# Kernel tuning notes

Measured on AMD Instinct MI355X. Metric: run time of the kernel, lower is better.

The kernel has to match this reference:

```python
import jax, jax.numpy as jnp
import numpy as np

S, E, K, D = 50000, 20000, 128, 128  # students, exercises, knowledge, emb dim
NE = 800000                          # edges per polarity
B = 8192                             # batch of response logs
L = 3                                # gcn layers
TEMP, CONTROL = 0.2, 0.3


def setup_inputs() -> dict:
    key = jax.random.key(0)
    ks = jax.random.split(key, 40)

    def nrm(i, shape, scale=0.05):
        return jax.random.normal(ks[i], shape, jnp.float32) * scale

    def uni(i, shape):
        return jax.random.uniform(ks[i], shape, jnp.float32)

    inp = {
        'stu_id': jax.random.randint(ks[0], (B,), 0, S, jnp.int32),
        'exer_id': jax.random.randint(ks[1], (B,), 0, E, jnp.int32),
        'kn_emb': uni(2, (B, K)),
        'ui1_u': jax.random.randint(ks[3], (NE,), 0, S, jnp.int32),
        'ui1_i': jax.random.randint(ks[4], (NE,), 0, E, jnp.int32),
        'ui1_val': uni(5, (NE,)), 'iu1_val': uni(6, (NE,)),
        'eps_ui1': uni(7, (NE,)), 'eps_iu1': uni(8, (NE,)),
        'ui0_u': jax.random.randint(ks[9], (NE,), 0, S, jnp.int32),
        'ui0_i': jax.random.randint(ks[10], (NE,), 0, E, jnp.int32),
        'ui0_val': uni(11, (NE,)), 'iu0_val': uni(12, (NE,)),
        'eps_ui0': uni(13, (NE,)), 'eps_iu0': uni(14, (NE,)),
        # embeddings
        'student_emb': nrm(15, (S, D)), 'exercise_emb': nrm(16, (E, D)),
        'knowledge_emb': nrm(17, (K, D)),
        'stu_b': nrm(18, (S, 1)), 'exer_b': nrm(19, (E, 1)), 'disc': nrm(20, (E, 1)),
        # edge-gate MLPs (polarity 1 and 0)
        'W1_l1': nrm(21, (D, 2 * D)), 'b1_l1': jnp.zeros((D,), jnp.float32),
        'W2_l1': nrm(22, (1, D)), 'b2_l1': jnp.zeros((1,), jnp.float32),
        'W1_l0': nrm(23, (D, 2 * D)), 'b1_l0': jnp.zeros((D,), jnp.float32),
        'W2_l0': nrm(24, (1, D)), 'b2_l0': jnp.zeros((1,), jnp.float32),
        # PosLinear prednet
        'pw1': nrm(25, (256, K)), 'pb1': jnp.zeros((256,), jnp.float32),
        'pw2': nrm(26, (128, 256)), 'pb2': jnp.zeros((128,), jnp.float32),
        'pw3': nrm(27, (1, 128)), 'pb3': jnp.zeros((1,), jnp.float32),
    }
    return inp


def _gate(uids, iids, uemb, iemb, W1, b1, W2, b2, eps):
    # concrete-distribution edge gate; embeddings are detached in original code
    row = jax.lax.stop_gradient(uemb)[uids]          # [NE, D]
    col = jax.lax.stop_gradient(iemb)[iids]          # [NE, D]
    h = jax.nn.relu(jnp.concatenate([row, col], axis=1) @ W1.T + b1)
    logit = (h @ W2.T + b2).reshape(-1)              # [NE]
    eps = jnp.clip(eps, 1e-6, 1.0 - 1e-6)
    g = jnp.log(eps) - jnp.log1p(-eps)               # logistic noise
    return CONTROL * jax.nn.sigmoid((logit + g) / TEMP) + (1.0 - CONTROL)


def _spmm(rows, cols, vals, x, n_rows):
    # out[rows] += vals * x[cols]
    return jax.ops.segment_sum(vals[:, None] * x[cols], rows, num_segments=n_rows)


def _poslin(x, W, b):
    Wp = 2.0 * jax.nn.relu(-W) + W  # == |W|
    return x @ Wp.T + b


def reference(stu_id, exer_id, kn_emb, ui1_u, ui1_i, ui1_val, iu1_val, eps_ui1,
              eps_iu1, ui0_u, ui0_i, ui0_val, iu0_val, eps_ui0, eps_iu0,
              student_emb, exercise_emb, knowledge_emb, stu_b, exer_b, disc,
              W1_l1, b1_l1, W2_l1, b2_l1, W1_l0, b1_l0, W2_l0, b2_l0,
              pw1, pb1, pw2, pb2, pw3, pb3):
    # --- graph_learner: per-edge gates on all 4 sparse matrices ---
    v_ui1 = ui1_val * _gate(ui1_u, ui1_i, student_emb, exercise_emb, W1_l1, b1_l1, W2_l1, b2_l1, eps_ui1)
    v_iu1 = iu1_val * _gate(ui1_u, ui1_i, student_emb, exercise_emb, W1_l1, b1_l1, W2_l1, b2_l1, eps_iu1)
    v_ui0 = ui0_val * _gate(ui0_u, ui0_i, student_emb, exercise_emb, W1_l0, b1_l0, W2_l0, b2_l0, eps_ui0)
    v_iu0 = iu0_val * _gate(ui0_u, ui0_i, student_emb, exercise_emb, W1_l0, b1_l0, W2_l0, b2_l0, eps_iu0)

    # --- graph_representations: L rounds of sparse propagation, mean over layers ---
    stu, exer = student_emb, exercise_emb
    stu_sum, exer_sum = stu, exer
    for _ in range(L):
        u1 = _spmm(ui1_u, ui1_i, v_ui1, exer, S)
        i1 = _spmm(ui1_i, ui1_u, v_iu1, stu, E)
        u0 = _spmm(ui0_u, ui0_i, v_ui0, exer, S)
        i0 = _spmm(ui0_i, ui0_u, v_iu0, stu, E)
        stu, exer = u1 + u0, i1 + i0
        stu_sum = stu_sum + stu
        exer_sum = exer_sum + exer
    stu_final = stu_sum / (L + 1)
    exer_final = exer_sum / (L + 1)

    # --- NCDM-style prediction head with PosLinear MLP ---
    stat = jax.nn.sigmoid(stu_final[stu_id] @ knowledge_emb.T + stu_b[stu_id])   # [B, K]
    diff = jax.nn.sigmoid(exer_final[exer_id] @ knowledge_emb.T + exer_b[exer_id])
    e_d = jax.nn.sigmoid(disc[exer_id])                                          # [B, 1]
    x = e_d * (stat - diff) * kn_emb
    h = jax.nn.sigmoid(_poslin(x, pw1, pb1))
    h = jax.nn.sigmoid(_poslin(h, pw2, pb2))
    out = jax.nn.sigmoid(_poslin(h, pw3, pb3)).reshape(-1)                       # [B]
    return out
```

## Files before the change

kernel.cpp:

```cpp
#include <hip/hip_runtime.h>
#include <hip/hip_bf16.h>
#include <math.h>

#define S_N 50000
#define E_N 20000
#define K_N 128
#define D_N 128
#define NE_N 800000
#define B_N 8192
#define L_N 3
#define GATE_TILES (NE_N / 64)
#define NB_S 782
#define NB_E 313
#define BPAD 464
#define BSLACK 480

typedef __attribute__((ext_vector_type(4))) float floatx4;
typedef __attribute__((ext_vector_type(8))) short short8v;

__device__ __forceinline__ unsigned short f2bf(float x) {
  unsigned int u = __float_as_uint(x);
  u += 0x7FFFu + ((u >> 16) & 1u);
  return (unsigned short)(u >> 16);
}
__device__ __forceinline__ float bf2f(unsigned short u) {
  return __uint_as_float(((unsigned int)u) << 16);
}
__device__ __forceinline__ float sigm(float z) { return 1.0f / (1.0f + __expf(-z)); }

__device__ __forceinline__ unsigned char f2e4m3(float x) {
  unsigned int u = __float_as_uint(x);
  unsigned char s = (unsigned char)((u >> 24) & 0x80);
  int e = (int)((u >> 23) & 0xFF) - 127;
  unsigned int m = u & 0x7FFFFF;
  if (((u >> 23) & 0xFF) == 0) return s;
  if (e >= 9) return s | 0x7E;
  if (e < -10) return s;
  if (e >= -6) {
    unsigned int keep = m >> 20;
    unsigned int rest = m & 0xFFFFF;
    if (rest > 0x80000u || (rest == 0x80000u && (keep & 1))) keep++;
    if (keep == 8) { keep = 0; e++; if (e >= 9) return s | 0x7E; }
    unsigned char b = (unsigned char)(s | ((e + 7) << 3) | keep);
    if ((b & 0x7F) == 0x7F) b = s | 0x7E;
    return b;
  }
  int shift = -6 - e;
  unsigned int full = 0x800000u | m;
  unsigned int q = full >> (20 + shift);
  unsigned int rest = full & ((1u << (20 + shift)) - 1);
  unsigned int half = 1u << (19 + shift);
  if (rest > half || (rest == half && (q & 1))) q++;
  if (q == 8) return s | 0x08;
  return (unsigned char)(s | q);
}
__device__ __forceinline__ unsigned int pk4_fp8(float4 v) {
  return (unsigned int)f2e4m3(v.x) | ((unsigned int)f2e4m3(v.y) << 8) |
         ((unsigned int)f2e4m3(v.z) << 16) | ((unsigned int)f2e4m3(v.w) << 24);
}

__global__ void prep_kernel(const float* __restrict__ W1_l1, const float* __restrict__ W1_l0,
                            const float* __restrict__ pw1, const float* __restrict__ pw2,
                            const float* __restrict__ pw3, const float* __restrict__ ke,
                            unsigned int* __restrict__ w1f8_1, unsigned int* __restrict__ w1f8_0,
                            float* __restrict__ pw1T, float* __restrict__ pw2T,
                            float* __restrict__ pw3a, float* __restrict__ keT) {
  int i = blockIdx.x * blockDim.x + threadIdx.x;
  if (i < 8192) { w1f8_1[i] = pk4_fp8(((const float4*)W1_l1)[i]); return; }
  i -= 8192;
  if (i < 8192) { w1f8_0[i] = pk4_fp8(((const float4*)W1_l0)[i]); return; }
  i -= 8192;
  if (i < 32768) { int d = i >> 8, j = i & 255; pw1T[i] = fabsf(pw1[j * 128 + d]); return; }
  i -= 32768;
  if (i < 32768) { int d = i >> 7, j = i & 127; pw2T[i] = fabsf(pw2[j * 256 + d]); return; }
  i -= 32768;
  if (i < 128) { pw3a[i] = fabsf(pw3[i]); return; }
  i -= 128;
  if (i < 16384) { int d = i >> 7, k = i & 127; keT[i] = ke[k * 128 + d]; return; }
}

__global__ void init_bf_kernel(const float* __restrict__ se, const float* __restrict__ ee,
                               unsigned short* __restrict__ sbf, unsigned short* __restrict__ ebf,
                               unsigned int* __restrict__ sf8, unsigned int* __restrict__ ef8,
                               float* __restrict__ sS, float* __restrict__ eS) {
  int i = blockIdx.x * blockDim.x + threadIdx.x;
  const int nS4 = S_N * 32, nE4 = E_N * 32;
  if (i < nS4) {
    float4 v = ((const float4*)se)[i];
    ((float4*)sS)[i] = v;
    unsigned int lo = (unsigned int)f2bf(v.x) | ((unsigned int)f2bf(v.y) << 16);
    unsigned int hi = (unsigned int)f2bf(v.z) | ((unsigned int)f2bf(v.w) << 16);
    ((uint2*)sbf)[i] = make_uint2(lo, hi);
    sf8[i] = pk4_fp8(v);
    return;
  }
  i -= nS4;
  if (i < nE4) {
    float4 v = ((const float4*)ee)[i];
    ((float4*)eS)[i] = v;
    unsigned int lo = (unsigned int)f2bf(v.x) | ((unsigned int)f2bf(v.y) << 16);
    unsigned int hi = (unsigned int)f2bf(v.z) | ((unsigned int)f2bf(v.w) << 16);
    ((uint2*)ebf)[i] = make_uint2(lo, hi);
    ef8[i] = pk4_fp8(v);
  }
}

__global__ void zero_kernel(int* __restrict__ p, int n) {
  int i = blockIdx.x * blockDim.x + threadIdx.x;
  if (i < n) p[i] = 0;
}

__global__ __launch_bounds__(256)
void histB_kernel(const int* __restrict__ u1, const int* __restrict__ i1,
                  const int* __restrict__ u0, const int* __restrict__ i0,
                  int* __restrict__ gHistS, int* __restrict__ gHistE) {
  __shared__ int hS[NB_S], hE[NB_E];
  int t = threadIdx.x;
  for (int b = t; b < NB_S; b += 256) hS[b] = 0;
  for (int b = t; b < NB_E; b += 256) hE[b] = 0;
  __syncthreads();
  int e0 = blockIdx.x * 2048;
  for (int k = 0; k < 8; ++k) {
    int e = e0 + k * 256 + t;
    if (e < NE_N) {
      atomicAdd(&hS[u1[e] >> 6], 1);
      atomicAdd(&hS[u0[e] >> 6], 1);
      atomicAdd(&hE[i1[e] >> 6], 1);
      atomicAdd(&hE[i0[e] >> 6], 1);
    }
  }
  __syncthreads();
  for (int b = t; b < NB_S; b += 256) if (hS[b]) atomicAdd(&gHistS[b], hS[b]);
  for (int b = t; b < NB_E; b += 256) if (hE[b]) atomicAdd(&gHistE[b], hE[b]);
}

__global__ __launch_bounds__(128)
void scanB_kernel(const int* __restrict__ gHistS, int* __restrict__ baseS,
                  int* __restrict__ gCurS, int* __restrict__ basePS,
                  const int* __restrict__ gHistE, int* __restrict__ baseE,
                  int* __restrict__ gCurE, int* __restrict__ basePE) {
  int w = threadIdx.x >> 6, l = threadIdx.x & 63;
  int n = w ? NB_E : NB_S;
  const int* src = w ? gHistE : gHistS;
  int* bs  = w ? baseE  : baseS;
  int* cur = w ? gCurE  : gCurS;
  int* bsP = w ? basePE : basePS;
  int carry = 0, carryP = 0;
  for (int base = 0; base < n; base += 64) {
    int i = base + l;
    int v = (i < n) ? src[i] : 0;
    int p = (i < n) ? ((v + BPAD + 15) & ~15) : 0;
    int x = v, y = p;
#pragma unroll
    for (int o = 1; o < 64; o <<= 1) {
      int xx = __shfl_up(x, o, 64);
      int yy = __shfl_up(y, o, 64);
      if (l >= o) { x += xx; y += yy; }
    }
    if (i < n) {
      int ex = carry + x - v;
      bs[i] = ex; cur[i] = ex;
      bsP[i] = carryP + y - p;
    }
    carry += __shfl(x, 63, 64);
    carryP += __shfl(y, 63, 64);
  }
  if (l == 0) { bs[n] = carry; bsP[n] = carryP; }
}

__global__ __launch_bounds__(256)
void append_kernel(const int* __restrict__ u1, const int* __restrict__ i1,
                   const int* __restrict__ u0, const int* __restrict__ i0,
                   const float* __restrict__ v_ui1, const float* __restrict__ v_iu1,
                   const float* __restrict__ v_ui0, const float* __restrict__ v_iu0,
                   int* __restrict__ gCurS, int* __restrict__ gCurE,
                   int2* __restrict__ recS, int2* __restrict__ recE) {
  __shared__ int hS[NB_S], hE[NB_E];
  int t = threadIdx.x;
  for (int b = t; b < NB_S; b += 256) hS[b] = 0;
  for (int b = t; b < NB_E; b += 256) hE[b] = 0;
  __syncthreads();
  int e0 = blockIdx.x * 2048;
  for (int k = 0; k < 8; ++k) {
    int e = e0 + k * 256 + t;
    if (e < NE_N) {
      atomicAdd(&hS[u1[e] >> 6], 1);
      atomicAdd(&hS[u0[e] >> 6], 1);
      atomicAdd(&hE[i1[e] >> 6], 1);
      atomicAdd(&hE[i0[e] >> 6], 1);
    }
  }
  __syncthreads();
  for (int b = t; b < NB_S; b += 256) { int c = hS[b]; hS[b] = c ? atomicAdd(&gCurS[b], c) : 0; }
  for (int b = t; b < NB_E; b += 256) { int c = hE[b]; hE[b] = c ? atomicAdd(&gCurE[b], c) : 0; }
  __syncthreads();
  for (int k = 0; k < 8; ++k) {
    int e = e0 + k * 256 + t;
    if (e < NE_N) {
      int a = u1[e], b = i1[e], c = u0[e], d = i0[e];
      int s;
      s = atomicAdd(&hS[a >> 6], 1); recS[s] = make_int2(((a & 63) << 16) | b, __float_as_int(v_ui1[e]));
      s = atomicAdd(&hE[b >> 6], 1); recE[s] = make_int2(((b & 63) << 16) | a, __float_as_int(v_iu1[e]));
      s = atomicAdd(&hS[c >> 6], 1); recS[s] = make_int2(((c & 63) << 16) | d, __float_as_int(v_ui0[e]));
      s = atomicAdd(&hE[d >> 6], 1); recE[s] = make_int2(((d & 63) << 16) | c, __float_as_int(v_iu0[e]));
    }
  }
}

__global__ __launch_bounds__(256)
void sortRow_kernel(const int* __restrict__ baseIn, const int* __restrict__ basePad,
                    const int2* __restrict__ rin_all, int2* __restrict__ rout_all,
                    int* __restrict__ rowPtr, int* __restrict__ rowCnt8, int nRowsTot) {
  __shared__ int cntR[64], offR[64], curR[64];
  int b = blockIdx.x, t = threadIdx.x;
  int bi = baseIn[b], cnt = baseIn[b + 1] - bi;
  int bo = basePad[b];
  int row0 = b * 64;
  const int2* rin = rin_all + bi;
  int2* rout = rout_all + bo;
  if (t < 64) cntR[t] = 0;
  __syncthreads();
  for (int j = t; j < cnt; j += 256) atomicAdd(&cntR[(rin[j].x >> 16) & 63], 1);
  __syncthreads();
  if (t < 64) {
    int p = (cntR[t] + 7) & ~7;
    int x = p;
#pragma unroll
    for (int o = 1; o < 64; o <<= 1) { int y = __shfl_up(x, o, 64); if (t >= o) x += y; }
    int ex = x - p;
    offR[t] = ex; curR[t] = ex;
    if (row0 + t < nRowsTot) {
      rowPtr[row0 + t] = bo + ex;
      rowCnt8[row0 + t] = p >> 3;
    }
  }
  __syncthreads();
  for (int j = t; j < cnt; j += 256) {
    int2 rc = rin[j];
    int r = (rc.x >> 16) & 63;
    int slot = atomicAdd(&curR[r], 1);
    rout[slot] = make_int2(rc.x & 0xFFFF, rc.y);
  }
  __syncthreads();
  if (t < 64) {
    int c = cntR[t], p = (c + 7) & ~7, o = offR[t];
    for (int j = c; j < p; ++j) rout[o + j] = make_int2(0, 0);
  }
}

__global__ __launch_bounds__(512, 2)
void gate_kernel(const int* __restrict__ eu, const int* __restrict__ ei,
                 const float* __restrict__ uival, const float* __restrict__ iuval,
                 const float* __restrict__ epsui, const float* __restrict__ epsiu,
                 const unsigned char* __restrict__ sf8, const unsigned char* __restrict__ ef8,
                 const unsigned char* __restrict__ w1f8,
                 const float* __restrict__ b1, const float* __restrict__ w2,
                 const float* __restrict__ b2,
                 float* __restrict__ vui, float* __restrict__ viu) {
  __shared__ unsigned char Xl[64 * 272];
  __shared__ float plds[8][16];
  int t = threadIdx.x;
  int wv = t >> 6, l = t & 63;
  int sub = l & 15, grp = l >> 4;
  int nh = wv & 1, rg = wv >> 1;

  long bfrag[4][8];
#pragma unroll
  for (int nt = 0; nt < 4; ++nt) {
    int col = nh * 64 + nt * 16 + sub;
#pragma unroll
    for (int ks = 0; ks < 8; ++ks)
      bfrag[nt][ks] = *(const long*)&w1f8[(col << 8) + ks * 32 + grp * 8];
  }
  float b1v[4], w2v[4];
#pragma unroll
  for (int nt = 0; nt < 4; ++nt) {
    int col = nh * 64 + nt * 16 + sub;
    b1v[nt] = b1[col];
    w2v[nt] = w2[col];
  }
  float b2s = b2[0];

  for (int tile = blockIdx.x; tile < GATE_TILES; tile += gridDim.x) {
    int e0 = tile * 64;
    {
      int el = t >> 3, q = t & 7;
      int eIdx = e0 + el;
      const unsigned char* srcrow = (q < 4)
          ? sf8 + (size_t)eu[eIdx] * 128 + q * 32
          : ef8 + (size_t)ei[eIdx] * 128 + (q - 4) * 32;
      uint4 c0 = ((const uint4*)srcrow)[0];
      uint4 c1 = ((const uint4*)srcrow)[1];
      *(uint4*)&Xl[el * 272 + q * 32] = c0;
      *(uint4*)&Xl[el * 272 + q * 32 + 16] = c1;
    }
    __syncthreads();

    floatx4 zero4 = {0.f, 0.f, 0.f, 0.f};
    floatx4 acc[4] = {zero4, zero4, zero4, zero4};
#pragma unroll
    for (int ks = 0; ks < 8; ++ks) {
      long a = *(const long*)&Xl[(rg * 16 + sub) * 272 + ks * 32 + grp * 8];
#pragma unroll
      for (int nt = 0; nt < 4; ++nt)
        acc[nt] = __builtin_amdgcn_mfma_f32_16x16x32_fp8_fp8(a, bfrag[nt][ks], acc[nt], 0, 0, 0);
    }
    float p0 = 0, p1 = 0, p2 = 0, p3 = 0;
#pragma unroll
    for (int nt = 0; nt < 4; ++nt) {
      float bb = b1v[nt], ww = w2v[nt];
      p0 += fmaxf(acc[nt][0] + bb, 0.0f) * ww;
      p1 += fmaxf(acc[nt][1] + bb, 0.0f) * ww;
      p2 += fmaxf(acc[nt][2] + bb, 0.0f) * ww;
      p3 += fmaxf(acc[nt][3] + bb, 0.0f) * ww;
    }
#pragma unroll
    for (int m = 1; m < 16; m <<= 1) {
      p0 += __shfl_xor(p0, m, 64);
      p1 += __shfl_xor(p1, m, 64);
      p2 += __shfl_xor(p2, m, 64);
      p3 += __shfl_xor(p3, m, 64);
    }
    if (sub < 4) {
      float pv = (sub == 0) ? p0 : (sub == 1) ? p1 : (sub == 2) ? p2 : p3;
      plds[wv][grp * 4 + sub] = pv;
    }
    __syncthreads();
    if (wv == 0) {
      float logit = plds[(l >> 4) * 2][l & 15] + plds[(l >> 4) * 2 + 1][l & 15] + b2s;
      int e = e0 + l;
      float ep = fminf(fmaxf(epsui[e], 1e-6f), 1.0f - 1e-6f);
      float g = __logf(ep) - log1pf(-ep);
      float s = 1.0f / (1.0f + __expf(-(logit + g) * 5.0f));
      vui[e] = uival[e] * (0.3f * s + 0.7f);
      ep = fminf(fmaxf(epsiu[e], 1e-6f), 1.0f - 1e-6f);
      g = __logf(ep) - log1pf(-ep);
      s = 1.0f / (1.0f + __expf(-(logit + g) * 5.0f));
      viu[e] = iuval[e] * (0.3f * s + 0.7f);
    }
    __syncthreads();
  }
}

__global__ __launch_bounds__(256)
void spmm_csr_kernel(const int* __restrict__ rowPtrS, const int* __restrict__ rowCnt8S,
                     const int2* __restrict__ rec2S,
                     const int* __restrict__ rowPtrE, const int* __restrict__ rowCnt8E,
                     const int2* __restrict__ rec2E,
                     const unsigned short* __restrict__ scur, const unsigned short* __restrict__ ecur,
                     unsigned short* __restrict__ snxt, unsigned short* __restrict__ enxt,
                     float* __restrict__ stuS, float* __restrict__ exeS) {
  int gw = (blockIdx.x * 256 + threadIdx.x) >> 6;
  int l = threadIdx.x & 63;
  int g = l >> 3, lane8 = l & 7;
  if (gw >= S_N + E_N) return;
  const int2* rec; const unsigned short* src; unsigned short* dst; float* sum;
  const int* rp; const int* rc8; int r;
  if (gw < S_N) { r = gw;       rp = rowPtrS; rc8 = rowCnt8S; rec = rec2S; src = ecur; dst = snxt; sum = stuS; }
  else          { r = gw - S_N; rp = rowPtrE; rc8 = rowCnt8E; rec = rec2E; src = scur; dst = enxt; sum = exeS; }
  int s0 = rp[r], n8 = rc8[r];
  float acc[16];
#pragma unroll
  for (int i = 0; i < 16; ++i) acc[i] = 0.f;
  for (int k = 0; k < n8; ++k) {
    int2 e = rec[s0 + k * 8 + g];
    float val = __int_as_float(e.y);
    const uint4* rowp = (const uint4*)(src + (size_t)e.x * 128);
    uint4 q0 = rowp[lane8 * 2];
    uint4 q1 = rowp[lane8 * 2 + 1];
#pragma unroll
    for (int i = 0; i < 4; ++i) {
      unsigned int w = ((const unsigned int*)&q0)[i];
      acc[2 * i]     = fmaf(val, bf2f((unsigned short)(w & 0xFFFF)), acc[2 * i]);
      acc[2 * i + 1] = fmaf(val, bf2f((unsigned short)(w >> 16)),    acc[2 * i + 1]);
    }
#pragma unroll
    for (int i = 0; i < 4; ++i) {
      unsigned int w = ((const unsigned int*)&q1)[i];
      acc[8 + 2 * i]     = fmaf(val, bf2f((unsigned short)(w & 0xFFFF)), acc[8 + 2 * i]);
      acc[8 + 2 * i + 1] = fmaf(val, bf2f((unsigned short)(w >> 16)),    acc[8 + 2 * i + 1]);
    }
  }
#pragma unroll
  for (int m = 8; m < 64; m <<= 1) {
#pragma unroll
    for (int i = 0; i < 16; ++i) acc[i] += __shfl_xor(acc[i], m, 64);
  }
  if (g == 0) {
    size_t base = (size_t)r * 128 + lane8 * 16;
    short8v o0, o1;
#pragma unroll
    for (int i = 0; i < 8; ++i) { o0[i] = (short)f2bf(acc[i]); o1[i] = (short)f2bf(acc[8 + i]); }
    *(short8v*)(dst + base) = o0;
    *(short8v*)(dst + base + 8) = o1;
    float4* sp = (float4*)(sum + base);
#pragma unroll
    for (int i = 0; i < 4; ++i) {
      float4 s = sp[i];
      s.x += acc[4 * i]; s.y += acc[4 * i + 1]; s.z += acc[4 * i + 2]; s.w += acc[4 * i + 3];
      sp[i] = s;
    }
  }
}

__global__ __launch_bounds__(256)
void head1_kernel(const int* __restrict__ stu_id, const int* __restrict__ exer_id,
                  const float* __restrict__ kn, const float* __restrict__ stuS,
                  const float* __restrict__ exeS, const float* __restrict__ keT,
                  const float* __restrict__ stub, const float* __restrict__ exeb,
                  const float* __restrict__ disc, float* __restrict__ xbuf) {
  __shared__ float srw[4][128], erw[4][128];
  int wv = threadIdx.x >> 6, l = threadIdx.x & 63;
  int b = blockIdx.x * 4 + wv;
  int sid = stu_id[b], eid = exer_id[b];
  float2 sv = ((const float2*)(stuS + (size_t)sid * 128))[l];
  float2 ev = ((const float2*)(exeS + (size_t)eid * 128))[l];
  srw[wv][2 * l] = sv.x * 0.25f; srw[wv][2 * l + 1] = sv.y * 0.25f;
  erw[wv][2 * l] = ev.x * 0.25f; erw[wv][2 * l + 1] = ev.y * 0.25f;
  __syncthreads();
  float s0 = 0, s1 = 0, d0 = 0, d1 = 0;
  for (int d = 0; d < 128; ++d) {
    float sd = srw[wv][d], ed = erw[wv][d];
    float ka = keT[d * 128 + l], kb = keT[d * 128 + l + 64];
    s0 = fmaf(sd, ka, s0); s1 = fmaf(sd, kb, s1);
    d0 = fmaf(ed, ka, d0); d1 = fmaf(ed, kb, d1);
  }
  float sbv = stub[sid], ebv = exeb[eid];
  float edv = sigm(disc[eid]);
  float st0 = sigm(s0 + sbv), st1 = sigm(s1 + sbv);
  float df0 = sigm(d0 + ebv), df1 = sigm(d1 + ebv);
  xbuf[(size_t)b * 128 + l]      = edv * (st0 - df0) * kn[(size_t)b * 128 + l];
  xbuf[(size_t)b * 128 + l + 64] = edv * (st1 - df1) * kn[(size_t)b * 128 + l + 64];
}

__global__ __launch_bounds__(256)
void head2_kernel(const float* __restrict__ xbuf, const float* __restrict__ pw1T,
                  const float* __restrict__ pb1, const float* __restrict__ pw2T,
                  const float* __restrict__ pb2, const float* __restrict__ pw3a,
                  const float* __restrict__ pb3, float* __restrict__ out) {
  __shared__ float xs[4][128], h1s[4][256], h2s[4][128];
  int wv = threadIdx.x >> 6, l = threadIdx.x & 63;
  int b = blockIdx.x * 4 + wv;
  xs[wv][l] = xbuf[(size_t)b * 128 + l];
  xs[wv][l + 64] = xbuf[(size_t)b * 128 + l + 64];
  __syncthreads();
#pragma unroll
  for (int q = 0; q < 4; ++q) {
    int j = q * 64 + l;
    float acc = 0.f;
    for (int d = 0; d < 128; ++d) acc = fmaf(xs[wv][d], pw1T[d * 256 + j], acc);
    h1s[wv][j] = sigm(acc + pb1[j]);
  }
  __syncthreads();
#pragma unroll
  for (int q = 0; q < 2; ++q) {
    int j = q * 64 + l;
    float acc = 0.f;
    for (int d = 0; d < 256; ++d) acc = fmaf(h1s[wv][d], pw2T[d * 128 + j], acc);
    h2s[wv][j] = sigm(acc + pb2[j]);
  }
  __syncthreads();
  float p = h2s[wv][l] * pw3a[l] + h2s[wv][l + 64] * pw3a[l + 64];
#pragma unroll
  for (int m = 1; m < 64; m <<= 1) p += __shfl_xor(p, m, 64);
  if (l == 0) out[b] = sigm(p + pb3[0]);
}

extern "C" void kernel_launch(void* const* d_in, const int* in_sizes, int n_in,
                              void* d_out, int out_size, void* d_ws, size_t ws_size,
                              hipStream_t stream) {
  const int*   stu_id  = (const int*)  d_in[0];
  const int*   exer_id = (const int*)  d_in[1];
  const float* kn_emb  = (const float*)d_in[2];
  const int*   ui1_u   = (const int*)  d_in[3];
  const int*   ui1_i   = (const int*)  d_in[4];
  const float* ui1_val = (const float*)d_in[5];
  const float* iu1_val = (const float*)d_in[6];
  const float* eps_ui1 = (const float*)d_in[7];
  const float* eps_iu1 = (const float*)d_in[8];
  const int*   ui0_u   = (const int*)  d_in[9];
  const int*   ui0_i   = (const int*)  d_in[10];
  const float* ui0_val = (const float*)d_in[11];
  const float* iu0_val = (const float*)d_in[12];
  const float* eps_ui0 = (const float*)d_in[13];
  const float* eps_iu0 = (const float*)d_in[14];
  const float* stu_emb = (const float*)d_in[15];
  const float* exe_emb = (const float*)d_in[16];
  const float* kno_emb = (const float*)d_in[17];
  const float* stu_b   = (const float*)d_in[18];
  const float* exe_b   = (const float*)d_in[19];
  const float* disc    = (const float*)d_in[20];
  const float* W1_l1   = (const float*)d_in[21];
  const float* b1_l1   = (const float*)d_in[22];
  const float* W2_l1   = (const float*)d_in[23];
  const float* b2_l1   = (const float*)d_in[24];
  const float* W1_l0   = (const float*)d_in[25];
  const float* b1_l0   = (const float*)d_in[26];
  const float* W2_l0   = (const float*)d_in[27];
  const float* b2_l0   = (const float*)d_in[28];
  const float* pw1     = (const float*)d_in[29];
  const float* pb1     = (const float*)d_in[30];
  const float* pw2     = (const float*)d_in[31];
  const float* pb2     = (const float*)d_in[32];
  const float* pw3     = (const float*)d_in[33];
  const float* pb3     = (const float*)d_in[34];
  float* out = (float*)d_out;
  (void)in_sizes; (void)n_in; (void)out_size; (void)ws_size;

  size_t off = 0;
  char* base = (char*)d_ws;
  auto carve = [&](size_t bytes) -> char* {
    char* p = base + off;
    off += (bytes + 255) & ~(size_t)255;
    return p;
  };
  unsigned int* w1f8_1 = (unsigned int*)carve(8192 * 4);
  unsigned int* w1f8_0 = (unsigned int*)carve(8192 * 4);
  float* pw1T = (float*)carve(32768 * 4);
  float* pw2T = (float*)carve(32768 * 4);
  float* pw3a = (float*)carve(128 * 4);
  float* keT  = (float*)carve(16384 * 4);
  float* v_ui1 = (float*)carve((size_t)2 * NE_N * 8 + (size_t)BSLACK * NB_S * 8);
  float* v_iu1 = v_ui1 + NE_N;
  float* v_ui0 = v_iu1 + NE_N;
  float* v_iu0 = v_ui0 + NE_N;
  unsigned short* stuBfA = (unsigned short*)carve((size_t)S_N * 128 * 2);
  unsigned short* stuBfB = (unsigned short*)carve((size_t)S_N * 128 * 2);
  unsigned short* exeBfA = (unsigned short*)carve((size_t)E_N * 128 * 2);
  unsigned short* exeBfB = (unsigned short*)carve((size_t)E_N * 128 * 2);
  unsigned int* sf8 = (unsigned int*)carve((size_t)S_N * 32 * 4);
  unsigned int* ef8 = (unsigned int*)carve((size_t)E_N * 32 * 4);
  float* stuS = (float*)carve((size_t)S_N * 128 * 4);
  float* exeS = (float*)carve((size_t)E_N * 128 * 4);
  int* gHistS = (int*)carve((size_t)(NB_S + NB_E) * 4);
  int* gHistE = gHistS + NB_S;
  int* baseSb  = (int*)carve((size_t)(NB_S + 1) * 4);
  int* baseEb  = (int*)carve((size_t)(NB_E + 1) * 4);
  int* basePSb = (int*)carve((size_t)(NB_S + 1) * 4);
  int* basePEb = (int*)carve((size_t)(NB_E + 1) * 4);
  int* gCurS  = (int*)carve((size_t)NB_S * 4);
  int* gCurE  = (int*)carve((size_t)NB_E * 4);
  int2* recS = (int2*)carve((size_t)2 * NE_N * 8 + (size_t)BSLACK * NB_E * 8);
  int2* recE = (int2*)carve((size_t)2 * NE_N * 8);
  int* rowPtrS  = (int*)carve((size_t)S_N * 4);
  int* rowCnt8S = (int*)carve((size_t)S_N * 4);
  int* rowPtrE  = (int*)carve((size_t)E_N * 4);
  int* rowCnt8E = (int*)carve((size_t)E_N * 4);
  float* xbuf = (float*)carve((size_t)B_N * 128 * 4);
  int2* rec2S = (int2*)v_ui1;
  int2* rec2E = recS;

  prep_kernel<<<(98432 + 255) / 256, 256, 0, stream>>>(W1_l1, W1_l0, pw1, pw2, pw3, kno_emb,
                                                       w1f8_1, w1f8_0, pw1T, pw2T, pw3a, keT);
  init_bf_kernel<<<(2240000 + 255) / 256, 256, 0, stream>>>(stu_emb, exe_emb, stuBfA, exeBfA,
                                                            sf8, ef8, stuS, exeS);
  zero_kernel<<<(NB_S + NB_E + 255) / 256, 256, 0, stream>>>(gHistS, NB_S + NB_E);
  histB_kernel<<<(NE_N + 2047) / 2048, 256, 0, stream>>>(ui1_u, ui1_i, ui0_u, ui0_i,
                                                         gHistS, gHistE);
  scanB_kernel<<<1, 128, 0, stream>>>(gHistS, baseSb, gCurS, basePSb,
                                      gHistE, baseEb, gCurE, basePEb);
  gate_kernel<<<2048, 512, 0, stream>>>(ui1_u, ui1_i, ui1_val, iu1_val, eps_ui1, eps_iu1,
                                        (const unsigned char*)sf8, (const unsigned char*)ef8,
                                        (const unsigned char*)w1f8_1, b1_l1, W2_l1, b2_l1,
                                        v_ui1, v_iu1);
  gate_kernel<<<2048, 512, 0, stream>>>(ui0_u, ui0_i, ui0_val, iu0_val, eps_ui0, eps_iu0,
                                        (const unsigned char*)sf8, (const unsigned char*)ef8,
                                        (const unsigned char*)w1f8_0, b1_l0, W2_l0, b2_l0,
                                        v_ui0, v_iu0);
  append_kernel<<<(NE_N + 2047) / 2048, 256, 0, stream>>>(ui1_u, ui1_i, ui0_u, ui0_i,
                                                          v_ui1, v_iu1, v_ui0, v_iu0,
                                                          gCurS, gCurE, recS, recE);
  sortRow_kernel<<<NB_S, 256, 0, stream>>>(baseSb, basePSb, recS, rec2S,
                                           rowPtrS, rowCnt8S, S_N);
  sortRow_kernel<<<NB_E, 256, 0, stream>>>(baseEb, basePEb, recE, rec2E,
                                           rowPtrE, rowCnt8E, E_N);
  const unsigned short* scur = stuBfA; const unsigned short* ecur = exeBfA;
  unsigned short* snxt = stuBfB; unsigned short* enxt = exeBfB;
  for (int layer = 0; layer < L_N; ++layer) {
    spmm_csr_kernel<<<(S_N + E_N + 3) / 4, 256, 0, stream>>>(
        rowPtrS, rowCnt8S, rec2S, rowPtrE, rowCnt8E, rec2E,
        scur, ecur, snxt, enxt, stuS, exeS);
    const unsigned short* t1 = scur; scur = snxt; snxt = (unsigned short*)t1;
    const unsigned short* t2 = ecur; ecur = enxt; enxt = (unsigned short*)t2;
  }
  head1_kernel<<<B_N / 4, 256, 0, stream>>>(stu_id, exer_id, kn_emb, stuS, exeS, keT,
                                            stu_b, exe_b, disc, xbuf);
  head2_kernel<<<B_N / 4, 256, 0, stream>>>(xbuf, pw1T, pb1, pw2T, pb2, pw3a, pb3, out);
}
```

Measured before the change: 748.9 us.

## Store GCN layer embeddings in FP8, merge gate launches, split gate epilogue

The propagation embeddings move from bf16 to e4m3 FP8 storage. This halves the bytes gathered per edge in the SpMM and lets the FP8 copies made for the gate serve as layer 0 directly, so the bf16 conversion is dropped. The two gate launches become one 4096-block launch that writes raw logits, and a separate elementwise kernel applies the concrete-distribution gating for all four edge sets. The risk is extra accuracy loss from FP8 rounding of intermediate layer embeddings, more software decode ALU work per element, and an extra round trip through global memory for the logits.

```diff
diff --git a/kernel.cpp b/kernel.cpp
--- a/kernel.cpp
+++ b/kernel.cpp
@@ -22,9 +22,6 @@
   unsigned int u = __float_as_uint(x);
   u += 0x7FFFu + ((u >> 16) & 1u);
   return (unsigned short)(u >> 16);
-}
-__device__ __forceinline__ float bf2f(unsigned short u) {
-  return __uint_as_float(((unsigned int)u) << 16);
 }
 __device__ __forceinline__ float sigm(float z) { return 1.0f / (1.0f + __expf(-z)); }
 
@@ -57,6 +54,13 @@
 __device__ __forceinline__ unsigned int pk4_fp8(float4 v) {
   return (unsigned int)f2e4m3(v.x) | ((unsigned int)f2e4m3(v.y) << 8) |
          ((unsigned int)f2e4m3(v.z) << 16) | ((unsigned int)f2e4m3(v.w) << 24);
+}
+__device__ __forceinline__ float e4m3f(unsigned char b) {
+  unsigned int m = b & 0x7F;
+  float fn = __uint_as_float((m << 20) + 0x3C000000u);
+  float fd = (float)m * 0.001953125f;
+  float mag = (m >= 8) ? fn : fd;
+  return (b & 0x80) ? -mag : mag;
 }
 
 __global__ void prep_kernel(const float* __restrict__ W1_l1, const float* __restrict__ W1_l0,
@@ -79,18 +83,14 @@
   if (i < 16384) { int d = i >> 7, k = i & 127; keT[i] = ke[k * 128 + d]; return; }
 }
 
-__global__ void init_bf_kernel(const float* __restrict__ se, const float* __restrict__ ee,
-                               unsigned short* __restrict__ sbf, unsigned short* __restrict__ ebf,
-                               unsigned int* __restrict__ sf8, unsigned int* __restrict__ ef8,
-                               float* __restrict__ sS, float* __restrict__ eS) {
+__global__ void init_kernel(const float* __restrict__ se, const float* __restrict__ ee,
+                            unsigned int* __restrict__ sf8, unsigned int* __restrict__ ef8,
+                            float* __restrict__ sS, float* __restrict__ eS) {
   int i = blockIdx.x * blockDim.x + threadIdx.x;
   const int nS4 = S_N * 32, nE4 = E_N * 32;
   if (i < nS4) {
     float4 v = ((const float4*)se)[i];
     ((float4*)sS)[i] = v;
-    unsigned int lo = (unsigned int)f2bf(v.x) | ((unsigned int)f2bf(v.y) << 16);
-    unsigned int hi = (unsigned int)f2bf(v.z) | ((unsigned int)f2bf(v.w) << 16);
-    ((uint2*)sbf)[i] = make_uint2(lo, hi);
     sf8[i] = pk4_fp8(v);
     return;
   }
@@ -98,9 +98,6 @@
   if (i < nE4) {
     float4 v = ((const float4*)ee)[i];
     ((float4*)eS)[i] = v;
-    unsigned int lo = (unsigned int)f2bf(v.x) | ((unsigned int)f2bf(v.y) << 16);
-    unsigned int hi = (unsigned int)f2bf(v.z) | ((unsigned int)f2bf(v.w) << 16);
-    ((uint2*)ebf)[i] = make_uint2(lo, hi);
     ef8[i] = pk4_fp8(v);
   }
 }
@@ -249,16 +246,25 @@
 }
 
 __global__ __launch_bounds__(512, 2)
-void gate_kernel(const int* __restrict__ eu, const int* __restrict__ ei,
-                 const float* __restrict__ uival, const float* __restrict__ iuval,
-                 const float* __restrict__ epsui, const float* __restrict__ epsiu,
+void gate_kernel(const int* __restrict__ eu1, const int* __restrict__ ei1,
+                 const int* __restrict__ eu0, const int* __restrict__ ei0,
                  const unsigned char* __restrict__ sf8, const unsigned char* __restrict__ ef8,
-                 const unsigned char* __restrict__ w1f8,
-                 const float* __restrict__ b1, const float* __restrict__ w2,
-                 const float* __restrict__ b2,
-                 float* __restrict__ vui, float* __restrict__ viu) {
+                 const unsigned char* __restrict__ w1f8_1, const unsigned char* __restrict__ w1f8_0,
+                 const float* __restrict__ b1_1, const float* __restrict__ w2_1,
+                 const float* __restrict__ b2_1,
+                 const float* __restrict__ b1_0, const float* __restrict__ w2_0,
+                 const float* __restrict__ b2_0,
+                 float* __restrict__ logit1, float* __restrict__ logit0) {
   __shared__ unsigned char Xl[64 * 272];
   __shared__ float plds[8][16];
+  const int* eu; const int* ei; const unsigned char* w1f8;
+  const float *b1p, *w2p, *b2p; float* lg;
+  if (blockIdx.x < 2048) {
+    eu = eu1; ei = ei1; w1f8 = w1f8_1; b1p = b1_1; w2p = w2_1; b2p = b2_1; lg = logit1;
+  } else {
+    eu = eu0; ei = ei0; w1f8 = w1f8_0; b1p = b1_0; w2p = w2_0; b2p = b2_0; lg = logit0;
+  }
+  int bb = blockIdx.x & 2047;
   int t = threadIdx.x;
   int wv = t >> 6, l = t & 63;
   int sub = l & 15, grp = l >> 4;
@@ -276,12 +282,12 @@
 #pragma unroll
   for (int nt = 0; nt < 4; ++nt) {
     int col = nh * 64 + nt * 16 + sub;
-    b1v[nt] = b1[col];
-    w2v[nt] = w2[col];
-  }
-  float b2s = b2[0];
-
-  for (int tile = blockIdx.x; tile < GATE_TILES; tile += gridDim.x) {
+    b1v[nt] = b1p[col];
+    w2v[nt] = w2p[col];
+  }
+  float b2s = b2p[0];
+
+  for (int tile = bb; tile < GATE_TILES; tile += 2048) {
     int e0 = tile * 64;
     {
       int el = t >> 3, q = t & 7;
@@ -308,11 +314,11 @@
     float p0 = 0, p1 = 0, p2 = 0, p3 = 0;
 #pragma unroll
     for (int nt = 0; nt < 4; ++nt) {
-      float bb = b1v[nt], ww = w2v[nt];
-      p0 += fmaxf(acc[nt][0] + bb, 0.0f) * ww;
-      p1 += fmaxf(acc[nt][1] + bb, 0.0f) * ww;
-      p2 += fmaxf(acc[nt][2] + bb, 0.0f) * ww;
-      p3 += fmaxf(acc[nt][3] + bb, 0.0f) * ww;
+      float bb2 = b1v[nt], ww = w2v[nt];
+      p0 += fmaxf(acc[nt][0] + bb2, 0.0f) * ww;
+      p1 += fmaxf(acc[nt][1] + bb2, 0.0f) * ww;
+      p2 += fmaxf(acc[nt][2] + bb2, 0.0f) * ww;
+      p3 += fmaxf(acc[nt][3] + bb2, 0.0f) * ww;
     }
 #pragma unroll
     for (int m = 1; m < 16; m <<= 1) {
@@ -326,20 +332,40 @@
       plds[wv][grp * 4 + sub] = pv;
     }
     __syncthreads();
-    if (wv == 0) {
-      float logit = plds[(l >> 4) * 2][l & 15] + plds[(l >> 4) * 2 + 1][l & 15] + b2s;
-      int e = e0 + l;
-      float ep = fminf(fmaxf(epsui[e], 1e-6f), 1.0f - 1e-6f);
-      float g = __logf(ep) - log1pf(-ep);
-      float s = 1.0f / (1.0f + __expf(-(logit + g) * 5.0f));
-      vui[e] = uival[e] * (0.3f * s + 0.7f);
-      ep = fminf(fmaxf(epsiu[e], 1e-6f), 1.0f - 1e-6f);
-      g = __logf(ep) - log1pf(-ep);
-      s = 1.0f / (1.0f + __expf(-(logit + g) * 5.0f));
-      viu[e] = iuval[e] * (0.3f * s + 0.7f);
-    }
+    if (wv == 0)
+      lg[e0 + l] = plds[(l >> 4) * 2][l & 15] + plds[(l >> 4) * 2 + 1][l & 15] + b2s;
     __syncthreads();
   }
+}
+
+__global__ __launch_bounds__(256)
+void gatefin_kernel(const float* __restrict__ logit1, const float* __restrict__ logit0,
+                    const float* __restrict__ ui1_val, const float* __restrict__ iu1_val,
+                    const float* __restrict__ eps_ui1, const float* __restrict__ eps_iu1,
+                    const float* __restrict__ ui0_val, const float* __restrict__ iu0_val,
+                    const float* __restrict__ eps_ui0, const float* __restrict__ eps_iu0,
+                    float* __restrict__ v_ui1, float* __restrict__ v_iu1,
+                    float* __restrict__ v_ui0, float* __restrict__ v_iu0) {
+  int e = blockIdx.x * 256 + threadIdx.x;
+  if (e >= NE_N) return;
+  float lg1 = logit1[e], lg0 = logit0[e];
+  float ep, g, s;
+  ep = fminf(fmaxf(eps_ui1[e], 1e-6f), 1.0f - 1e-6f);
+  g = __logf(ep) - log1pf(-ep);
+  s = 1.0f / (1.0f + __expf(-(lg1 + g) * 5.0f));
+  v_ui1[e] = ui1_val[e] * (0.3f * s + 0.7f);
+  ep = fminf(fmaxf(eps_iu1[e], 1e-6f), 1.0f - 1e-6f);
+  g = __logf(ep) - log1pf(-ep);
+  s = 1.0f / (1.0f + __expf(-(lg1 + g) * 5.0f));
+  v_iu1[e] = iu1_val[e] * (0.3f * s + 0.7f);
+  ep = fminf(fmaxf(eps_ui0[e], 1e-6f), 1.0f - 1e-6f);
+  g = __logf(ep) - log1pf(-ep);
+  s = 1.0f / (1.0f + __expf(-(lg0 + g) * 5.0f));
+  v_ui0[e] = ui0_val[e] * (0.3f * s + 0.7f);
+  ep = fminf(fmaxf(eps_iu0[e], 1e-6f), 1.0f - 1e-6f);
+  g = __logf(ep) - log1pf(-ep);
+  s = 1.0f / (1.0f + __expf(-(lg0 + g) * 5.0f));
+  v_iu0[e] = iu0_val[e] * (0.3f * s + 0.7f);
 }
 
 __global__ __launch_bounds__(256)
@@ -347,14 +373,14 @@
                      const int2* __restrict__ rec2S,
                      const int* __restrict__ rowPtrE, const int* __restrict__ rowCnt8E,
                      const int2* __restrict__ rec2E,
-                     const unsigned short* __restrict__ scur, const unsigned short* __restrict__ ecur,
-                     unsigned short* __restrict__ snxt, unsigned short* __restrict__ enxt,
+                     const unsigned char* __restrict__ scur, const unsigned char* __restrict__ ecur,
+                     unsigned char* __restrict__ snxt, unsigned char* __restrict__ enxt,
                      float* __restrict__ stuS, float* __restrict__ exeS) {
   int gw = (blockIdx.x * 256 + threadIdx.x) >> 6;
   int l = threadIdx.x & 63;
   int g = l >> 3, lane8 = l & 7;
   if (gw >= S_N + E_N) return;
-  const int2* rec; const unsigned short* src; unsigned short* dst; float* sum;
+  const int2* rec; const unsigned char* src; unsigned char* dst; float* sum;
   const int* rp; const int* rc8; int r;
   if (gw < S_N) { r = gw;       rp = rowPtrS; rc8 = rowCnt8S; rec = rec2S; src = ecur; dst = snxt; sum = stuS; }
   else          { r = gw - S_N; rp = rowPtrE; rc8 = rowCnt8E; rec = rec2E; src = scur; dst = enxt; sum = exeS; }
@@ -365,20 +391,15 @@
   for (int k = 0; k < n8; ++k) {
     int2 e = rec[s0 + k * 8 + g];
     float val = __int_as_float(e.y);
-    const uint4* rowp = (const uint4*)(src + (size_t)e.x * 128);
-    uint4 q0 = rowp[lane8 * 2];
-    uint4 q1 = rowp[lane8 * 2 + 1];
+    uint4 q = ((const uint4*)(src + (size_t)e.x * 128))[lane8];
+    unsigned int ws[4] = {q.x, q.y, q.z, q.w};
 #pragma unroll
     for (int i = 0; i < 4; ++i) {
-      unsigned int w = ((const unsigned int*)&q0)[i];
-      acc[2 * i]     = fmaf(val, bf2f((unsigned short)(w & 0xFFFF)), acc[2 * i]);
-      acc[2 * i + 1] = fmaf(val, bf2f((unsigned short)(w >> 16)),    acc[2 * i + 1]);
-    }
-#pragma unroll
-    for (int i = 0; i < 4; ++i) {
-      unsigned int w = ((const unsigned int*)&q1)[i];
-      acc[8 + 2 * i]     = fmaf(val, bf2f((unsigned short)(w & 0xFFFF)), acc[8 + 2 * i]);
-      acc[8 + 2 * i + 1] = fmaf(val, bf2f((unsigned short)(w >> 16)),    acc[8 + 2 * i + 1]);
+      unsigned int w = ws[i];
+      acc[4 * i]     = fmaf(val, e4m3f((unsigned char)(w        & 0xFF)), acc[4 * i]);
+      acc[4 * i + 1] = fmaf(val, e4m3f((unsigned char)((w >> 8)  & 0xFF)), acc[4 * i + 1]);
+      acc[4 * i + 2] = fmaf(val, e4m3f((unsigned char)((w >> 16) & 0xFF)), acc[4 * i + 2]);
+      acc[4 * i + 3] = fmaf(val, e4m3f((unsigned char)((w >> 24) & 0xFF)), acc[4 * i + 3]);
     }
   }
 #pragma unroll
@@ -387,13 +408,14 @@
     for (int i = 0; i < 16; ++i) acc[i] += __shfl_xor(acc[i], m, 64);
   }
   if (g == 0) {
-    size_t base = (size_t)r * 128 + lane8 * 16;
-    short8v o0, o1;
-#pragma unroll
-    for (int i = 0; i < 8; ++i) { o0[i] = (short)f2bf(acc[i]); o1[i] = (short)f2bf(acc[8 + i]); }
-    *(short8v*)(dst + base) = o0;
-    *(short8v*)(dst + base + 8) = o1;
-    float4* sp = (float4*)(sum + base);
+    size_t cbase = (size_t)r * 128 + lane8 * 16;
+    uint4 o;
+    o.x = pk4_fp8(make_float4(acc[0], acc[1], acc[2], acc[3]));
+    o.y = pk4_fp8(make_float4(acc[4], acc[5], acc[6], acc[7]));
+    o.z = pk4_fp8(make_float4(acc[8], acc[9], acc[10], acc[11]));
+    o.w = pk4_fp8(make_float4(acc[12], acc[13], acc[14], acc[15]));
+    *(uint4*)(dst + cbase) = o;
+    float4* sp = (float4*)(sum + cbase);
 #pragma unroll
     for (int i = 0; i < 4; ++i) {
       float4 s = sp[i];
@@ -524,14 +546,14 @@
   float* v_iu1 = v_ui1 + NE_N;
   float* v_ui0 = v_iu1 + NE_N;
   float* v_iu0 = v_ui0 + NE_N;
-  unsigned short* stuBfA = (unsigned short*)carve((size_t)S_N * 128 * 2);
-  unsigned short* stuBfB = (unsigned short*)carve((size_t)S_N * 128 * 2);
-  unsigned short* exeBfA = (unsigned short*)carve((size_t)E_N * 128 * 2);
-  unsigned short* exeBfB = (unsigned short*)carve((size_t)E_N * 128 * 2);
-  unsigned int* sf8 = (unsigned int*)carve((size_t)S_N * 32 * 4);
-  unsigned int* ef8 = (unsigned int*)carve((size_t)E_N * 32 * 4);
+  unsigned int* sf8A = (unsigned int*)carve((size_t)S_N * 32 * 4);
+  unsigned int* sf8B = (unsigned int*)carve((size_t)S_N * 32 * 4);
+  unsigned int* ef8A = (unsigned int*)carve((size_t)E_N * 32 * 4);
+  unsigned int* ef8B = (unsigned int*)carve((size_t)E_N * 32 * 4);
   float* stuS = (float*)carve((size_t)S_N * 128 * 4);
   float* exeS = (float*)carve((size_t)E_N * 128 * 4);
+  float* logit1 = (float*)carve((size_t)NE_N * 4);
+  float* logit0 = (float*)carve((size_t)NE_N * 4);
   int* gHistS = (int*)carve((size_t)(NB_S + NB_E) * 4);
   int* gHistE = gHistS + NB_S;
   int* baseSb  = (int*)carve((size_t)(NB_S + 1) * 4);
@@ -552,21 +574,22 @@
 
   prep_kernel<<<(98432 + 255) / 256, 256, 0, stream>>>(W1_l1, W1_l0, pw1, pw2, pw3, kno_emb,
                                                        w1f8_1, w1f8_0, pw1T, pw2T, pw3a, keT);
-  init_bf_kernel<<<(2240000 + 255) / 256, 256, 0, stream>>>(stu_emb, exe_emb, stuBfA, exeBfA,
-                                                            sf8, ef8, stuS, exeS);
+  init_kernel<<<(2240000 + 255) / 256, 256, 0, stream>>>(stu_emb, exe_emb, sf8A, ef8A,
+                                                         stuS, exeS);
   zero_kernel<<<(NB_S + NB_E + 255) / 256, 256, 0, stream>>>(gHistS, NB_S + NB_E);
   histB_kernel<<<(NE_N + 2047) / 2048, 256, 0, stream>>>(ui1_u, ui1_i, ui0_u, ui0_i,
                                                          gHistS, gHistE);
   scanB_kernel<<<1, 128, 0, stream>>>(gHistS, baseSb, gCurS, basePSb,
                                       gHistE, baseEb, gCurE, basePEb);
-  gate_kernel<<<2048, 512, 0, stream>>>(ui1_u, ui1_i, ui1_val, iu1_val, eps_ui1, eps_iu1,
-                                        (const unsigned char*)sf8, (const unsigned char*)ef8,
-                                        (const unsigned char*)w1f8_1, b1_l1, W2_l1, b2_l1,
-                                        v_ui1, v_iu1);
-  gate_kernel<<<2048, 512, 0, stream>>>(ui0_u, ui0_i, ui0_val, iu0_val, eps_ui0, eps_iu0,
-                                        (const unsigned char*)sf8, (const unsigned char*)ef8,
-                                        (const unsigned char*)w1f8_0, b1_l0, W2_l0, b2_l0,
-                                        v_ui0, v_iu0);
+  gate_kernel<<<4096, 512, 0, stream>>>(ui1_u, ui1_i, ui0_u, ui0_i,
+                                        (const unsigned char*)sf8A, (const unsigned char*)ef8A,
+                                        (const unsigned char*)w1f8_1, (const unsigned char*)w1f8_0,
+                                        b1_l1, W2_l1, b2_l1, b1_l0, W2_l0, b2_l0,
+                                        logit1, logit0);
+  gatefin_kernel<<<(NE_N + 255) / 256, 256, 0, stream>>>(logit1, logit0,
+                                                         ui1_val, iu1_val, eps_ui1, eps_iu1,
+                                                         ui0_val, iu0_val, eps_ui0, eps_iu0,
+                                                         v_ui1, v_iu1, v_ui0, v_iu0);
   append_kernel<<<(NE_N + 2047) / 2048, 256, 0, stream>>>(ui1_u, ui1_i, ui0_u, ui0_i,
                                                           v_ui1, v_iu1, v_ui0, v_iu0,
                                                           gCurS, gCurE, recS, recE);
@@ -574,14 +597,16 @@
                                            rowPtrS, rowCnt8S, S_N);
   sortRow_kernel<<<NB_E, 256, 0, stream>>>(baseEb, basePEb, recE, rec2E,
                                            rowPtrE, rowCnt8E, E_N);
-  const unsigned short* scur = stuBfA; const unsigned short* ecur = exeBfA;
-  unsigned short* snxt = stuBfB; unsigned short* enxt = exeBfB;
+  const unsigned char* scur = (const unsigned char*)sf8A;
+  const unsigned char* ecur = (const unsigned char*)ef8A;
+  unsigned char* snxt = (unsigned char*)sf8B;
+  unsigned char* enxt = (unsigned char*)ef8B;
   for (int layer = 0; layer < L_N; ++layer) {
     spmm_csr_kernel<<<(S_N + E_N + 3) / 4, 256, 0, stream>>>(
         rowPtrS, rowCnt8S, rec2S, rowPtrE, rowCnt8E, rec2E,
         scur, ecur, snxt, enxt, stuS, exeS);
-    const unsigned short* t1 = scur; scur = snxt; snxt = (unsigned short*)t1;
-    const unsigned short* t2 = ecur; ecur = enxt; enxt = (unsigned short*)t2;
+    const unsigned char* t1 = scur; scur = snxt; snxt = (unsigned char*)t1;
+    const unsigned char* t2 = ecur; ecur = enxt; enxt = (unsigned char*)t2;
   }
   head1_kernel<<<B_N / 4, 256, 0, stream>>>(stu_id, exer_id, kn_emb, stuS, exeS, keT,
                                             stu_b, exe_b, disc, xbuf);
```

Result: slower. 994.8 us (+32.8%).
